# Kernel optimization log

Measured on AMD Instinct MI355X. Metric: run time of the kernel, lower is better.

The kernel has to match this reference:

```python
import jax, jax.numpy as jnp
import numpy as np

N_GROUP = 64
GROUP_SIZE = 64
INPUT_DIM = 2048
BATCH = 8192
N_MONTN = 512


def setup_inputs() -> dict:
    key = jax.random.key(0)
    k1, k2, k3, k4, k5 = jax.random.split(key, 5)
    x = jax.random.normal(k1, (BATCH, INPUT_DIM), dtype=jnp.float32)
    weight = jax.random.normal(k2, (N_GROUP * GROUP_SIZE, INPUT_DIM), dtype=jnp.float32) * 0.02
    bias = jax.random.normal(k3, (N_GROUP * GROUP_SIZE,), dtype=jnp.float32) * 0.02
    rand_u = jax.random.uniform(k4, (BATCH,), dtype=jnp.float32)
    montn_index = jax.random.randint(k5, (N_MONTN,), 0, INPUT_DIM, dtype=jnp.int32)
    return {"x": x, "weight": weight, "bias": bias, "rand_u": rand_u,
            "montn_index": montn_index}


def reference(x, weight, bias, rand_u, montn_index):
    # Square the weights on monotone input columns (in-place in torch).
    w = weight.at[:, montn_index].set(weight[:, montn_index] ** 2)
    # y = x @ w^T + b  -> [B, n_group * n_group_size]
    y = jnp.einsum('bi,oi->bo', x, w) + bias
    B = y.shape[0]
    # per-group min over contiguous slices, then max over groups
    group_mins = y.reshape(B, N_GROUP, GROUP_SIZE).min(axis=2)  # [B, n_group]
    out = group_mins.max(axis=1)                                 # [B]
    # vectorized Bernoulli: 1.0 if u < sigmoid(out) else 0.0
    sample = (rand_u < jax.nn.sigmoid(out)).astype(jnp.float32)
    return sample.reshape(-1, 1)
```

## Files before the change

### kernel.cpp

```cpp
#include <hip/hip_runtime.h>
#include <cmath>


typedef _Float16 f16x8 __attribute__((ext_vector_type(8)));
typedef float f32x4 __attribute__((ext_vector_type(4)));

#define MARGIN_EPS 4e-3f
#define MAX_UNDEC 96

__device__ __forceinline__ void async_load16(const void* gptr, void* lptr) {
  __builtin_amdgcn_global_load_lds(
      (const __attribute__((address_space(1))) void*)gptr,
      (__attribute__((address_space(3))) void*)lptr, 16, 0, 0);
}

__device__ __forceinline__ float us2f(unsigned short u) {
  return (float)__builtin_bit_cast(_Float16, u);
}

__global__ void convert_split(float* __restrict__ x, float* __restrict__ wgt,
                              const int* __restrict__ montn,
                              int* __restrict__ count) {
  __shared__ unsigned msk[64];
  const int t = threadIdx.x, l = t & 63, w = t >> 6;
  const int r = blockIdx.x * 4 + w;
  const int use_mask = (r >= 8192) ? 1 : 0;
  if (blockIdx.x == 0 && t == 0) *count = 0;
  if (use_mask) {
    if (t < 64) msk[t] = 0u;
    __syncthreads();
    for (int j = t; j < 512; j += 256) {
      const int c = montn[j];
      atomicOr(&msk[c >> 5], 1u << (c & 31));
    }
    __syncthreads();
  }
  float* rowp = use_mask ? (wgt + (size_t)(r - 8192) * 2048)
                         : (x + (size_t)r * 2048);
  float4 v[8];
#pragma unroll
  for (int j = 0; j < 8; ++j) v[j] = ((const float4*)rowp)[l + 64 * j];
  unsigned mw[8];
#pragma unroll
  for (int j = 0; j < 8; ++j)
    mw[j] = use_mask ? msk[(l >> 3) + 8 * j] : 0u;

  unsigned short* up = (unsigned short*)rowp;
#pragma unroll
  for (int j = 0; j < 8; ++j) {
    unsigned short hs[4], ls[4];
    const float* fv = (const float*)&v[j];
#pragma unroll
    for (int c = 0; c < 4; ++c) {
      float f = fv[c];
      if ((mw[j] >> (4 * (l & 7) + c)) & 1u) f = f * f;
      _Float16 h = (_Float16)f;
      float res = f - (float)h;
      _Float16 lo = (_Float16)res;
      hs[c] = __builtin_bit_cast(unsigned short, h);
      ls[c] = __builtin_bit_cast(unsigned short, lo);
    }
    uint2 H, L;
    H.x = (unsigned)hs[0] | ((unsigned)hs[1] << 16);
    H.y = (unsigned)hs[2] | ((unsigned)hs[3] << 16);
    L.x = (unsigned)ls[0] | ((unsigned)ls[1] << 16);
    L.y = (unsigned)ls[2] | ((unsigned)ls[3] << 16);
    *((uint2*)(up + 4 * l + 256 * j)) = H;
    *((uint2*)(up + 2048 + 4 * l + 256 * j)) = L;
  }
}

__global__ __launch_bounds__(256, 4) void gemm_minmax(
    const unsigned short* __restrict__ X, const unsigned short* __restrict__ W,
    const float* __restrict__ bias, float* __restrict__ gmins) {
  __shared__ unsigned short As[2 * 128 * 32];
  __shared__ unsigned short Bs[2 * 128 * 32];
  const int t = threadIdx.x;
  const int lane = t & 63;
  const int w = t >> 6;
  const int wm = w >> 1, wn = w & 1;
  const int lin = blockIdx.x;
  const int sid = lin >> 3;
  const int m0 = (sid >> 2) * 128;
  const int n0 = ((lin & 7) * 4 + (sid & 3)) * 128;

  const int rowS = w * 16 + (lane >> 2);
  const int gch = (((lane & 3) ^ ((lane >> 2) & 3)) * 8);
  size_t sA[2], sB[2];
#pragma unroll
  for (int c = 0; c < 2; ++c) {
    sA[c] = (size_t)(m0 + c * 64 + rowS) * 4096 + gch;
    sB[c] = (size_t)(n0 + c * 64 + rowS) * 4096 + gch;
  }

  const int am = lane & 15, quad = lane >> 4;
  int aoff[4], boff[4];
#pragma unroll
  for (int i = 0; i < 4; ++i) {
    const int ar = wm * 64 + i * 16 + am;
    const int br = wn * 64 + i * 16 + am;
    aoff[i] = ar * 32 + ((quad ^ (am & 3)) * 8);
    boff[i] = br * 32 + ((quad ^ (am & 3)) * 8);
  }

  f32x4 acc[4][4];
#pragma unroll
  for (int i = 0; i < 4; ++i)
#pragma unroll
    for (int j = 0; j < 4; ++j) acc[i][j] = (f32x4){0.f, 0.f, 0.f, 0.f};

#pragma unroll
  for (int c = 0; c < 2; ++c) {
    async_load16(X + sA[c], As + c * 2048 + w * 512);
    async_load16(W + sB[c], Bs + c * 2048 + w * 512);
  }

#pragma unroll 1
  for (int it = 0; it < 64; ++it) {
    const int buf = it & 1;
    __syncthreads();
    if (it + 1 < 64) {
      const int kin = (it + 1) * 32;
      const int ob = (buf ^ 1) * 4096;
#pragma unroll
      for (int c = 0; c < 2; ++c) {
        async_load16(X + sA[c] + kin, As + ob + c * 2048 + w * 512);
        async_load16(W + sB[c] + kin, Bs + ob + c * 2048 + w * 512);
      }
    }
    const unsigned short* Ab = As + buf * 4096;
    const unsigned short* Bb = Bs + buf * 4096;
    f16x8 av[4], bv[4];
#pragma unroll
    for (int i = 0; i < 4; ++i) av[i] = *(const f16x8*)(Ab + aoff[i]);
#pragma unroll
    for (int i = 0; i < 4; ++i) bv[i] = *(const f16x8*)(Bb + boff[i]);
#pragma unroll
    for (int mb = 0; mb < 4; ++mb)
#pragma unroll
      for (int nb = 0; nb < 4; ++nb)
        acc[mb][nb] = __builtin_amdgcn_mfma_f32_16x16x32_f16(
            av[mb], bv[nb], acc[mb][nb], 0, 0, 0);
  }

  float bv4[4];
#pragma unroll
  for (int nb = 0; nb < 4; ++nb) bv4[nb] = bias[n0 + wn * 64 + nb * 16 + am];
  const int grp = (n0 >> 6) + wn;
#pragma unroll
  for (int mb = 0; mb < 4; ++mb) {
#pragma unroll
    for (int reg = 0; reg < 4; ++reg) {
      float v = fminf(fminf(acc[mb][0][reg] + bv4[0], acc[mb][1][reg] + bv4[1]),
                      fminf(acc[mb][2][reg] + bv4[2], acc[mb][3][reg] + bv4[3]));
      v = fminf(v, __shfl_xor(v, 1, 64));
      v = fminf(v, __shfl_xor(v, 2, 64));
      v = fminf(v, __shfl_xor(v, 4, 64));
      v = fminf(v, __shfl_xor(v, 8, 64));
      if (am == 0) {
        const int row = m0 + wm * 64 + mb * 16 + quad * 4 + reg;
        gmins[(size_t)row * 64 + grp] = v;
      }
    }
  }
}

__global__ void finalize_margin(const float* __restrict__ gmins,
                                const float* __restrict__ rand_u,
                                float* __restrict__ out,
                                int* __restrict__ count, int* __restrict__ undec,
                                float4* __restrict__ ybuf4) {
  if (blockIdx.x < 384)
    ybuf4[(size_t)blockIdx.x * 256 + threadIdx.x] = (float4){0.f, 0.f, 0.f, 0.f};
  const int wv = threadIdx.x >> 6, lane = threadIdx.x & 63;
  const int row = blockIdx.x * 4 + wv;
  float v = gmins[(size_t)row * 64 + lane];
  v = fmaxf(v, __shfl_xor(v, 1, 64));
  v = fmaxf(v, __shfl_xor(v, 2, 64));
  v = fmaxf(v, __shfl_xor(v, 4, 64));
  v = fmaxf(v, __shfl_xor(v, 8, 64));
  v = fmaxf(v, __shfl_xor(v, 16, 64));
  v = fmaxf(v, __shfl_xor(v, 32, 64));
  if (lane == 0) {
    const float u = rand_u[row];
    const float slo = 1.0f / (1.0f + expf(-(v - MARGIN_EPS)));
    const float shi = 1.0f / (1.0f + expf(-(v + MARGIN_EPS)));
    if (u < slo) {
      out[row] = 1.0f;
    } else if (u >= shi) {
      out[row] = 0.0f;
    } else {
      const int i = atomicAdd(count, 1);
      if (i < 8192) undec[i] = row;
    }
  }
}

__global__ __launch_bounds__(256) void recompute_rows(
    const unsigned short* __restrict__ X, const unsigned short* __restrict__ W,
    const int* __restrict__ count, const int* __restrict__ undec,
    float* __restrict__ ybuf) {
  __shared__ float wf[64 * 129];
  __shared__ float part[256];
  const int g = blockIdx.x, kc = blockIdx.y;
  const int t = threadIdx.x;
  int n = *count;
  if (n > MAX_UNDEC) n = MAX_UNDEC;
  if (n == 0) return;

  {
    const int cl = t >> 2, ks = t & 3;
    const unsigned short* wp =
        W + (size_t)(g * 64 + cl) * 4096 + kc * 128 + ks * 32;
    float* dst = wf + cl * 129 + ks * 32;
#pragma unroll
    for (int i = 0; i < 32; i += 8) {
      uint4 hv = *(const uint4*)(wp + i);
      uint4 lv = *(const uint4*)(wp + 2048 + i);
      const unsigned* hw = (const unsigned*)&hv;
      const unsigned* lw = (const unsigned*)&lv;
#pragma unroll
      for (int m = 0; m < 4; ++m) {
        dst[i + 2 * m] = us2f((unsigned short)(hw[m] & 0xFFFF)) +
                         us2f((unsigned short)(lw[m] & 0xFFFF));
        dst[i + 2 * m + 1] = us2f((unsigned short)(hw[m] >> 16)) +
                             us2f((unsigned short)(lw[m] >> 16));
      }
    }
  }
  __syncthreads();

  const int col = t & 63, kq = t >> 6;
  const float* wcol = wf + col * 129 + kq * 32;
  for (int s = 0; s < n; ++s) {
    const int row = undec[s];
    const unsigned short* xp = X + (size_t)row * 4096 + kc * 128 + kq * 32;
    float acc = 0.f;
#pragma unroll
    for (int i = 0; i < 32; i += 8) {
      uint4 hv = *(const uint4*)(xp + i);
      uint4 lv = *(const uint4*)(xp + 2048 + i);
      const unsigned* hw = (const unsigned*)&hv;
      const unsigned* lw = (const unsigned*)&lv;
#pragma unroll
      for (int m = 0; m < 4; ++m) {
        const float x0 = us2f((unsigned short)(hw[m] & 0xFFFF)) +
                         us2f((unsigned short)(lw[m] & 0xFFFF));
        const float x1 = us2f((unsigned short)(hw[m] >> 16)) +
                         us2f((unsigned short)(lw[m] >> 16));
        acc = fmaf(x0, wcol[i + 2 * m], acc);
        acc = fmaf(x1, wcol[i + 2 * m + 1], acc);
      }
    }
    part[t] = acc;
    __syncthreads();
    if (t < 64) {
      const float y = part[t] + part[t + 64] + part[t + 128] + part[t + 192];
      atomicAdd(ybuf + (size_t)s * 4096 + g * 64 + t, y);
    }
    __syncthreads();
  }
}

__global__ void decide(const float* __restrict__ ybuf,
                       const int* __restrict__ undec, const int* __restrict__ count,
                       const float* __restrict__ bias,
                       const float* __restrict__ rand_u, float* __restrict__ out) {
  __shared__ float gm[64];
  int n = *count;
  if (n > MAX_UNDEC) n = MAX_UNDEC;
  const int s = blockIdx.x;
  if (s >= n) return;
  const int t = threadIdx.x;
  const int g = t >> 2, p4 = t & 3;
  const float* yb = ybuf + (size_t)s * 4096;
  const int c0 = g * 64 + p4 * 16;
  float m = 3.4e38f;
#pragma unroll
  for (int e = 0; e < 16; ++e) m = fminf(m, yb[c0 + e] + bias[c0 + e]);
  m = fminf(m, __shfl_xor(m, 1, 64));
  m = fminf(m, __shfl_xor(m, 2, 64));
  if (p4 == 0) gm[g] = m;
  __syncthreads();
  if (t < 64) {
    float v = gm[t];
    v = fmaxf(v, __shfl_xor(v, 1, 64));
    v = fmaxf(v, __shfl_xor(v, 2, 64));
    v = fmaxf(v, __shfl_xor(v, 4, 64));
    v = fmaxf(v, __shfl_xor(v, 8, 64));
    v = fmaxf(v, __shfl_xor(v, 16, 64));
    v = fmaxf(v, __shfl_xor(v, 32, 64));
    if (t == 0) {
      const int row = undec[s];
      const float sg = 1.0f / (1.0f + expf(-v));
      out[row] = (rand_u[row] < sg) ? 1.0f : 0.0f;
    }
  }
}

extern "C" void kernel_launch(void* const* d_in, const int* in_sizes, int n_in,
                              void* d_out, int out_size, void* d_ws, size_t ws_size,
                              hipStream_t stream) {
  float* x = (float*)d_in[0];
  float* weight = (float*)d_in[1];
  const float* bias = (const float*)d_in[2];
  const float* rand_u = (const float*)d_in[3];
  const int* montn = (const int*)d_in[4];
  float* out = (float*)d_out;

  char* ws = (char*)d_ws;
  int* count = (int*)ws;
  int* undec = (int*)(ws + 256);
  float* ybuf = (float*)(ws + 65536);
  float* gmins = (float*)(ws + 65536 + 1572864);

  convert_split<<<3072, 256, 0, stream>>>(x, weight, montn, count);
  gemm_minmax<<<2048, 256, 0, stream>>>(
      (const unsigned short*)x, (const unsigned short*)weight, bias, gmins);
  finalize_margin<<<2048, 256, 0, stream>>>(gmins, rand_u, out, count, undec,
                                            (float4*)ybuf);
  recompute_rows<<<dim3(64, 16), 256, 0, stream>>>(
      (const unsigned short*)x, (const unsigned short*)weight, count, undec, ybuf);
  decide<<<MAX_UNDEC, 256, 0, stream>>>(ybuf, undec, count, bias, rand_u, out);
}
```

Before: 321.9 us.

## Replace double-buffered K=32 pipeline with single-buffered K=64 tiles

The GEMM main loop now loads 64-wide K tiles into a single LDS buffer per iteration, halving the iteration count, and uses an 8-way XOR swizzle instead of a 4-way one. The point is to amortise barrier and loop overhead over twice as many MFMAs per iteration. In exchange, the prefetch overlap of the double buffer is lost: each iteration waits for its loads before computing, which could expose global memory latency unless the other resident blocks hide it.

```diff
diff --git a/kernel.cpp b/kernel.cpp
--- a/kernel.cpp
+++ b/kernel.cpp
@@ -73,8 +73,8 @@
 __global__ __launch_bounds__(256, 4) void gemm_minmax(
     const unsigned short* __restrict__ X, const unsigned short* __restrict__ W,
     const float* __restrict__ bias, float* __restrict__ gmins) {
-  __shared__ unsigned short As[2 * 128 * 32];
-  __shared__ unsigned short Bs[2 * 128 * 32];
+  __shared__ unsigned short As[128 * 64];
+  __shared__ unsigned short Bs[128 * 64];
   const int t = threadIdx.x;
   const int lane = t & 63;
   const int w = t >> 6;
@@ -84,24 +84,32 @@
   const int m0 = (sid >> 2) * 128;
   const int n0 = ((lin & 7) * 4 + (sid & 3)) * 128;
 
-  const int rowS = w * 16 + (lane >> 2);
-  const int gch = (((lane & 3) ^ ((lane >> 2) & 3)) * 8);
-  size_t sA[2], sB[2];
-#pragma unroll
-  for (int c = 0; c < 2; ++c) {
-    sA[c] = (size_t)(m0 + c * 64 + rowS) * 4096 + gch;
-    sB[c] = (size_t)(n0 + c * 64 + rowS) * 4096 + gch;
+  const int rowBase = w * 8 + (lane >> 3);
+  const int gchunk = ((lane & 7) ^ ((lane >> 3) & 7)) * 8;
+  size_t sA[4], sB[4];
+#pragma unroll
+  for (int c = 0; c < 4; ++c) {
+    sA[c] = (size_t)(m0 + c * 32 + rowBase) * 4096 + gchunk;
+    sB[c] = (size_t)(n0 + c * 32 + rowBase) * 4096 + gchunk;
+  }
+  unsigned short* ldsA[4];
+  unsigned short* ldsB[4];
+#pragma unroll
+  for (int c = 0; c < 4; ++c) {
+    ldsA[c] = As + c * 2048 + w * 512;
+    ldsB[c] = Bs + c * 2048 + w * 512;
   }
 
   const int am = lane & 15, quad = lane >> 4;
-  int aoff[4], boff[4];
+  int arow[4], brow[4];
 #pragma unroll
   for (int i = 0; i < 4; ++i) {
-    const int ar = wm * 64 + i * 16 + am;
-    const int br = wn * 64 + i * 16 + am;
-    aoff[i] = ar * 32 + ((quad ^ (am & 3)) * 8);
-    boff[i] = br * 32 + ((quad ^ (am & 3)) * 8);
-  }
+    arow[i] = (wm * 64 + i * 16 + am) * 64;
+    brow[i] = (wn * 64 + i * 16 + am) * 64;
+  }
+  int swz[2];
+#pragma unroll
+  for (int h = 0; h < 2; ++h) swz[h] = (((h << 2) + quad) ^ (am & 7)) * 8;
 
   f32x4 acc[4][4];
 #pragma unroll
@@ -109,38 +117,31 @@
 #pragma unroll
     for (int j = 0; j < 4; ++j) acc[i][j] = (f32x4){0.f, 0.f, 0.f, 0.f};
 
-#pragma unroll
-  for (int c = 0; c < 2; ++c) {
-    async_load16(X + sA[c], As + c * 2048 + w * 512);
-    async_load16(W + sB[c], Bs + c * 2048 + w * 512);
-  }
-
 #pragma unroll 1
-  for (int it = 0; it < 64; ++it) {
-    const int buf = it & 1;
-    __syncthreads();
-    if (it + 1 < 64) {
-      const int kin = (it + 1) * 32;
-      const int ob = (buf ^ 1) * 4096;
-#pragma unroll
-      for (int c = 0; c < 2; ++c) {
-        async_load16(X + sA[c] + kin, As + ob + c * 2048 + w * 512);
-        async_load16(W + sB[c] + kin, Bs + ob + c * 2048 + w * 512);
-      }
-    }
-    const unsigned short* Ab = As + buf * 4096;
-    const unsigned short* Bb = Bs + buf * 4096;
-    f16x8 av[4], bv[4];
-#pragma unroll
-    for (int i = 0; i < 4; ++i) av[i] = *(const f16x8*)(Ab + aoff[i]);
-#pragma unroll
-    for (int i = 0; i < 4; ++i) bv[i] = *(const f16x8*)(Bb + boff[i]);
-#pragma unroll
-    for (int mb = 0; mb < 4; ++mb)
-#pragma unroll
-      for (int nb = 0; nb < 4; ++nb)
-        acc[mb][nb] = __builtin_amdgcn_mfma_f32_16x16x32_f16(
-            av[mb], bv[nb], acc[mb][nb], 0, 0, 0);
+  for (int it = 0; it < 32; ++it) {
+    const int kin = it * 64;
+    __syncthreads();
+#pragma unroll
+    for (int c = 0; c < 4; ++c) {
+      async_load16(X + sA[c] + kin, ldsA[c]);
+      async_load16(W + sB[c] + kin, ldsB[c]);
+    }
+    __syncthreads();
+
+#pragma unroll
+    for (int h = 0; h < 2; ++h) {
+      f16x8 av[4], bv[4];
+#pragma unroll
+      for (int i = 0; i < 4; ++i) av[i] = *(const f16x8*)(As + arow[i] + swz[h]);
+#pragma unroll
+      for (int i = 0; i < 4; ++i) bv[i] = *(const f16x8*)(Bs + brow[i] + swz[h]);
+#pragma unroll
+      for (int mb = 0; mb < 4; ++mb)
+#pragma unroll
+        for (int nb = 0; nb < 4; ++nb)
+          acc[mb][nb] = __builtin_amdgcn_mfma_f32_16x16x32_f16(
+              av[mb], bv[nb], acc[mb][nb], 0, 0, 0);
+    }
   }
 
   float bv4[4];
```

After: 291.0 us. 9.6% less time.
